# Performance work log

Hardware: AMD Instinct MI355X
Metric: run time of the kernel (lower is better)

## Reference

```python
import jax, jax.numpy as jnp
import numpy as np

N, E = 50000, 800000
D, H, C, ED = 128, 8, 16, 32  # in_channels, heads, head_dim, edge_dim
EPS = 1e-5

def _ln(x, g, b):
    mu = jnp.mean(x, axis=-1, keepdims=True)
    var = jnp.mean((x - mu) ** 2, axis=-1, keepdims=True)
    return (x - mu) * jax.lax.rsqrt(var + EPS) * g + b

def setup_inputs() -> dict:
    key = jax.random.key(0)
    ks = jax.random.split(key, 20)
    s = 0.05
    inp = {
        'x': jax.random.normal(ks[0], (N, D), jnp.float32),
        'edge_index': jax.random.randint(ks[1], (2, E), 0, N, jnp.int64),
        'edge_attr': jax.random.normal(ks[2], (E, ED), jnp.float32),
        'Wq': jax.random.normal(ks[3], (D, H * C)) * s,
        'bq': jnp.zeros((H * C,)),
        'Wk': jax.random.normal(ks[4], (D, H * C)) * s,
        'bk': jnp.zeros((H * C,)),
        'Wv': jax.random.normal(ks[5], (D, H * C)) * s,
        'bv': jnp.zeros((H * C,)),
        'We': jax.random.normal(ks[6], (ED, H * C)) * s,
        'Wskip': jax.random.normal(ks[7], (D, H * C)) * s,
        'bskip': jnp.zeros((H * C,)),
        'ln1_g': jnp.ones((D,)), 'ln1_b': jnp.zeros((D,)),
        'W1': jax.random.normal(ks[8], (D, 4 * D)) * s,
        'b1': jnp.zeros((4 * D,)),
        'W2': jax.random.normal(ks[9], (4 * D, D)) * s,
        'b2': jnp.zeros((D,)),
        'ln2_g': jnp.ones((D,)), 'ln2_b': jnp.zeros((D,)),
    }
    return inp

def reference(x, edge_index, edge_attr, Wq, bq, Wk, bk, Wv, bv, We, Wskip, bskip,
              ln1_g, ln1_b, W1, b1, W2, b2, ln2_g, ln2_b):
    src, dst = edge_index[0], edge_index[1]
    # node-level projections, then gather per-edge  [N,H,C] -> [E,H,C]
    q = (x @ Wq + bq).reshape(N, H, C)
    k = (x @ Wk + bk).reshape(N, H, C)
    v = (x @ Wv + bv).reshape(N, H, C)
    e = (edge_attr @ We).reshape(E, H, C)
    k_e = k[src] + e
    alpha = jnp.sum(q[dst] * k_e, axis=-1) / jnp.sqrt(jnp.float32(C))  # [E,H]
    # segment softmax over destination nodes
    m = jax.ops.segment_max(alpha, dst, num_segments=N)               # [N,H]
    p = jnp.exp(alpha - m[dst])
    denom = jax.ops.segment_sum(p, dst, num_segments=N)
    a = p / (denom[dst] + 1e-16)
    out_e = (v[src] + e) * a[..., None]                               # [E,H,C]
    attn = jax.ops.segment_sum(out_e, dst, num_segments=N).reshape(N, H * C)
    attn = attn + x @ Wskip + bskip  # root/skip connection
    # transformer block: residual + LN + FFN + LN (dropout = identity, eval)
    h = _ln(x + attn, ln1_g, ln1_b)
    ffn = jax.nn.relu(h @ W1 + b1) @ W2 + b2
    return _ln(h + ffn, ln2_g, ln2_b)
```

## Files before the change

kernel.cpp:

```cpp
#include <hip/hip_runtime.h>
#include <hip/hip_bf16.h>

using bf16 = __hip_bfloat16;
typedef __attribute__((ext_vector_type(8))) short short8;
typedef __attribute__((ext_vector_type(4))) float floatx4;

#define NN 50000
#define EE 800000
#define DD 128
#define HH 8
#define CC 16
#define EDD 32
#define DF 512
#define NQC 64
#define PART 782

__device__ __forceinline__ float b2f(bf16 v) { return __bfloat162float(v); }
__device__ __forceinline__ float bs2f(short s) {
    bf16 h = *reinterpret_cast<bf16*>(&s);
    return __bfloat162float(h);
}
__device__ __forceinline__ float bu2f(unsigned short s) {
    unsigned int u = ((unsigned int)s) << 16;
    return *reinterpret_cast<float*>(&u);
}
__device__ __forceinline__ short f2bs(float v) {
    bf16 h = __float2bfloat16(v);
    return *reinterpret_cast<short*>(&h);
}

__device__ __forceinline__ int clampn(int v)
{
    return (v < 0) ? 0 : (v >= NN ? NN - 1 : v);
}

__global__ void k_packall(const float* __restrict__ Wq, const float* __restrict__ Wk,
                          const float* __restrict__ Wv, const float* __restrict__ Wsk,
                          const float* __restrict__ W1, const float* __restrict__ W2,
                          const float* __restrict__ We,
                          bf16* __restrict__ wqp, bf16* __restrict__ wkp,
                          bf16* __restrict__ wvp, bf16* __restrict__ wskp,
                          bf16* __restrict__ w1p, bf16* __restrict__ w2p,
                          bf16* __restrict__ wep,
                          const int* __restrict__ ei, int* __restrict__ flag)
{
    int idx = blockIdx.x * 256 + threadIdx.x;
    const float* W; bf16* out; int ksteps, N, local;
    if (idx < 65536) {
        int wsel = idx >> 14; local = idx & 16383;
        W   = (wsel == 0) ? Wq  : (wsel == 1) ? Wk  : (wsel == 2) ? Wv  : Wsk;
        out = (wsel == 0) ? wqp : (wsel == 1) ? wkp : (wsel == 2) ? wvp : wskp;
        ksteps = 4; N = 128;
    } else if (idx < 131072) { local = idx - 65536;  W = W1; out = w1p; ksteps = 4;  N = 512; }
    else if (idx < 196608)   { local = idx - 131072; W = W2; out = w2p; ksteps = 16; N = 128; }
    else if (idx < 200704)   { local = idx - 196608; W = We; out = wep; ksteps = 1;  N = 128; }
    else {
        if (idx == 200704) {
            int all0 = 1;
            for (int i = 0; i < 16; ++i) all0 &= (ei[2 * i + 1] == 0);
            flag[0] = all0;
        }
        return;
    }
    int j = local & 7, lane = (local >> 3) & 63, rest = local >> 9;
    int kstep = rest % ksteps, ntile = rest / ksteps;
    int quad = lane >> 4, m = lane & 15;
    int k = kstep * 32 + quad * 8 + j;
    int n = ntile * 16 + m;
    out[local] = __float2bfloat16(W[(size_t)k * N + n]);
}

__global__ __launch_bounds__(256) void k_proj(
    const float* __restrict__ x,
    const bf16* __restrict__ wqp, const bf16* __restrict__ wkp,
    const bf16* __restrict__ wvp, const bf16* __restrict__ wskp,
    const float* __restrict__ bq, const float* __restrict__ bk,
    const float* __restrict__ bv, const float* __restrict__ bsk,
    bf16* __restrict__ qb, unsigned int* __restrict__ kvb,
    bf16* __restrict__ skipb)
{
    __shared__ __align__(16) short xs[32][136];
    __shared__ __align__(16) short os[32][520];
    const int t = threadIdx.x;
    const int wave = t >> 6, lane = t & 63;
    const int quad = lane >> 4, m = lane & 15;
    const int n0 = blockIdx.x * 32;

    for (int idx = t; idx < 32 * 32; idx += 256) {
        int row = idx >> 5, g = idx & 31;
        int node = n0 + row;
        float4 xv = {0.f, 0.f, 0.f, 0.f};
        if (node < NN) xv = *reinterpret_cast<const float4*>(&x[(size_t)node * 128 + g * 4]);
        short4 s4;
        s4.x = f2bs(xv.x); s4.y = f2bs(xv.y); s4.z = f2bs(xv.z); s4.w = f2bs(xv.w);
        *reinterpret_cast<short4*>(&xs[row][g * 4]) = s4;
    }
    __syncthreads();

    const bf16* Wp = (wave == 0) ? wqp : (wave == 1) ? wkp : (wave == 2) ? wvp : wskp;
    const float* bias = (wave == 0) ? bq : (wave == 1) ? bk : (wave == 2) ? bv : bsk;

    floatx4 acc[2][8];
#pragma unroll
    for (int mt = 0; mt < 2; ++mt)
#pragma unroll
        for (int nt = 0; nt < 8; ++nt) acc[mt][nt] = (floatx4){0.f, 0.f, 0.f, 0.f};

#pragma unroll
    for (int kstep = 0; kstep < 4; ++kstep) {
        short8 af0 = *reinterpret_cast<const short8*>(&xs[m][kstep * 32 + quad * 8]);
        short8 af1 = *reinterpret_cast<const short8*>(&xs[16 + m][kstep * 32 + quad * 8]);
#pragma unroll
        for (int nt = 0; nt < 8; ++nt) {
            short8 bf = *reinterpret_cast<const short8*>(
                reinterpret_cast<const short*>(Wp) + ((nt * 4 + kstep) * 64 + lane) * 8);
            acc[0][nt] = __builtin_amdgcn_mfma_f32_16x16x32_bf16(af0, bf, acc[0][nt], 0, 0, 0);
            acc[1][nt] = __builtin_amdgcn_mfma_f32_16x16x32_bf16(af1, bf, acc[1][nt], 0, 0, 0);
        }
    }
#pragma unroll
    for (int nt = 0; nt < 8; ++nt) {
        float bs = bias[nt * 16 + m];
#pragma unroll
        for (int mt = 0; mt < 2; ++mt)
#pragma unroll
            for (int r = 0; r < 4; ++r)
                os[mt * 16 + quad * 4 + r][wave * 128 + nt * 16 + m] = f2bs(acc[mt][nt][r] + bs);
    }
    __syncthreads();
    for (int idx = t; idx < 32 * 64; idx += 256) {
        int row = idx >> 6, c = idx & 63;
        int node = n0 + row;
        if (node >= NN) continue;
        unsigned int qu  = *reinterpret_cast<const unsigned int*>(&os[row][2 * c]);
        unsigned int ku  = *reinterpret_cast<const unsigned int*>(&os[row][128 + 2 * c]);
        unsigned int vu  = *reinterpret_cast<const unsigned int*>(&os[row][256 + 2 * c]);
        unsigned int sku = *reinterpret_cast<const unsigned int*>(&os[row][384 + 2 * c]);
        reinterpret_cast<unsigned int*>(qb)[(size_t)node * 64 + c] = qu;
        reinterpret_cast<unsigned int*>(skipb)[(size_t)node * 64 + c] = sku;
        uint2 kv;
        kv.x = (ku & 0xffffu) | (vu << 16);
        kv.y = (ku >> 16) | (vu & 0xffff0000u);
        reinterpret_cast<uint2*>(kvb)[(size_t)node * 64 + c] = kv;
    }
}

__global__ void k_hist(const int* __restrict__ ei, const int* __restrict__ flag,
                       int* __restrict__ deg)
{
    int tt = blockIdx.x * 256 + threadIdx.x;
    int i0 = tt * 2;
    if (i0 >= EE) return;
    int d0, d1;
    if (flag[0]) {
        int4 v = *reinterpret_cast<const int4*>(&ei[2 * EE + 2 * i0]);
        d0 = v.x; d1 = v.z;
    } else {
        int2 v = *reinterpret_cast<const int2*>(&ei[EE + i0]);
        d0 = v.x; d1 = v.y;
    }
    atomicAdd(&deg[clampn(d0)], 1);
    atomicAdd(&deg[clampn(d1)], 1);
}

__global__ __launch_bounds__(1024) void k_scan(const int* __restrict__ deg,
                                               int* __restrict__ rowstart)
{
    __shared__ int s[1024];
    const int t = threadIdx.x;
    const int CH = 49;
    int base = t * CH;
    int sum = 0;
    for (int i = 0; i < CH; i++) {
        int idx = base + i;
        if (idx < NN) sum += deg[idx];
    }
    s[t] = sum;
    __syncthreads();
    int own = sum;
    for (int off = 1; off < 1024; off <<= 1) {
        int v = (t >= off) ? s[t - off] : 0;
        __syncthreads();
        s[t] += v;
        __syncthreads();
    }
    int run = s[t] - own;
    for (int i = 0; i < CH; i++) {
        int idx = base + i;
        if (idx < NN) {
            rowstart[idx] = run;
            run += deg[idx];
        }
    }
    if (t == 0) rowstart[NN] = EE;
}

__global__ void k_scatter(const int* __restrict__ ei, const int* __restrict__ flag,
                          const int* __restrict__ rowstart,
                          int* __restrict__ cursor, int* __restrict__ srcs,
                          const float* __restrict__ ea,
                          short* __restrict__ eacsr)
{
    int i = blockIdx.x * 256 + threadIdx.x;
    if (i >= EE) return;
    int is64 = flag[0];
    int d = clampn(is64 ? ei[2 * EE + 2 * i] : ei[EE + i]);
    int s = clampn(is64 ? ei[2 * i] : ei[i]);
    int pos = rowstart[d] + atomicAdd(&cursor[d], 1);
    __builtin_nontemporal_store(s, &srcs[pos]);
    const float4* er = reinterpret_cast<const float4*>(ea + (size_t)i * 32);
    short8* dst = reinterpret_cast<short8*>(eacsr + (size_t)pos * 32);
#pragma unroll
    for (int g = 0; g < 4; ++g) {
        float4 a = er[2 * g], b = er[2 * g + 1];
        short8 o;
        o[0] = f2bs(a.x); o[1] = f2bs(a.y); o[2] = f2bs(a.z); o[3] = f2bs(a.w);
        o[4] = f2bs(b.x); o[5] = f2bs(b.y); o[6] = f2bs(b.z); o[7] = f2bs(b.w);
        __builtin_nontemporal_store(o, &dst[g]);
    }
}

__global__ __launch_bounds__(256) void k_attn(
    const float* __restrict__ x,
    const short* __restrict__ eacsr, const bf16* __restrict__ wep,
    const bf16* __restrict__ qb, const unsigned int* __restrict__ kvb,
    const bf16* __restrict__ skipb,
    const int* __restrict__ rowstart, const int* __restrict__ srcs,
    const float* __restrict__ ln1g, const float* __restrict__ ln1b,
    int* __restrict__ qcounter, bf16* __restrict__ hb)
{
    __shared__ __align__(16) short es[4][128][18];
    __shared__ __align__(16) short wes[4096];
    const int t = threadIdx.x;
    const int wave = t >> 6, lane = t & 63;
    const int quad = lane >> 4, m = lane & 15;

    for (int idx = t; idx < 512; idx += 256)
        *reinterpret_cast<short8*>(&wes[idx * 8]) =
            *reinterpret_cast<const short8*>(reinterpret_cast<const short*>(wep) + idx * 8);
    __syncthreads();

    short (*esw)[18] = es[wave];
    const float QS = 0.3606737602f;

    const int gw = blockIdx.x * 4 + wave;
    const int c  = gw & (NQC - 1);
    const int base = c * PART;
    const int cnt_c = (NN - base < PART) ? (NN - base) : PART;
    int* qc = qcounter + c * 16;

    for (;;) {
        int nl;
        if (lane == 0) nl = atomicAdd(qc, 4);
        nl = __builtin_amdgcn_readfirstlane(nl);
        if (nl >= cnt_c) break;
        const int nhi = (nl + 4 < cnt_c) ? nl + 4 : cnt_c;

        for (int ni = nl; ni < nhi; ++ni) {
            const int n = base + ni;

            unsigned int qp = reinterpret_cast<const unsigned int*>(qb)[(size_t)n * 64 + lane];
            float q0 = bu2f((unsigned short)(qp & 0xffffu)) * QS;
            float q1 = bu2f((unsigned short)(qp >> 16)) * QS;

            const int eoff = rowstart[n], eend = rowstart[n + 1];
            float lsum = 0.f, acc0 = 0.f, acc1 = 0.f;

            for (int p0 = eoff; p0 < eend; p0 += 16) {
                int pos = p0 + m;
                int pc = (pos < eend) ? pos : eoff;
                int sj_all = srcs[pc];

                short8 Af = *reinterpret_cast<const short8*>(eacsr + (size_t)pc * 32 + quad * 8);

                uint2 kvr[16];
#pragma unroll
                for (int j = 0; j < 16; ++j) {
                    int sj = __builtin_amdgcn_readlane(sj_all, j);
                    kvr[j] = reinterpret_cast<const uint2*>(kvb + (size_t)(unsigned)sj * 128)[lane];
                }

#pragma unroll
                for (int nt = 0; nt < 8; ++nt) {
                    short8 Bf = *reinterpret_cast<const short8*>(&wes[(nt * 64 + lane) * 8]);
                    floatx4 C = {0.f, 0.f, 0.f, 0.f};
                    C = __builtin_amdgcn_mfma_f32_16x16x32_bf16(Af, Bf, C, 0, 0, 0);
                    int col = nt * 16 + m;
                    unsigned int d0 = (unsigned int)(unsigned short)f2bs(C[0]) |
                                      ((unsigned int)(unsigned short)f2bs(C[1]) << 16);
                    unsigned int d1 = (unsigned int)(unsigned short)f2bs(C[2]) |
                                      ((unsigned int)(unsigned short)f2bs(C[3]) << 16);
                    unsigned int* p = reinterpret_cast<unsigned int*>(&esw[col][quad * 4]);
                    p[0] = d0; p[1] = d1;
                }
                __builtin_amdgcn_wave_barrier();

                unsigned int ear[8], ebr[8];
                {
                    const unsigned int* ra = reinterpret_cast<const unsigned int*>(&esw[2 * lane][0]);
                    const unsigned int* rb = reinterpret_cast<const unsigned int*>(&esw[2 * lane + 1][0]);
#pragma unroll
                    for (int jj = 0; jj < 8; ++jj) { ear[jj] = ra[jj]; ebr[jj] = rb[jj]; }
                }

                int cnt = eend - p0; if (cnt > 16) cnt = 16;
#pragma unroll
                for (int j = 0; j < 16; ++j) {
                    unsigned int eva = ear[j >> 1], evb = ebr[j >> 1];
                    float e0 = (j & 1) ? bu2f((unsigned short)(eva >> 16))
                                       : bu2f((unsigned short)(eva & 0xffffu));
                    float e1 = (j & 1) ? bu2f((unsigned short)(evb >> 16))
                                       : bu2f((unsigned short)(evb & 0xffffu));
                    float k0 = bu2f((unsigned short)(kvr[j].x & 0xffffu));
                    float v0 = bu2f((unsigned short)(kvr[j].x >> 16));
                    float k1 = bu2f((unsigned short)(kvr[j].y & 0xffffu));
                    float v1 = bu2f((unsigned short)(kvr[j].y >> 16));
                    float pr = fmaf(k1 + e1, q1, (k0 + e0) * q0);
                    pr += __int_as_float(__builtin_amdgcn_ds_swizzle(__float_as_int(pr), 0x041F));
                    pr += __int_as_float(__builtin_amdgcn_ds_swizzle(__float_as_int(pr), 0x081F));
                    pr += __int_as_float(__builtin_amdgcn_ds_swizzle(__float_as_int(pr), 0x101F));
                    float w = (j < cnt) ? __builtin_amdgcn_exp2f(pr) : 0.f;
                    lsum += w;
                    acc0 = fmaf(v0 + e0, w, acc0);
                    acc1 = fmaf(v1 + e1, w, acc1);
                }
                __builtin_amdgcn_wave_barrier();
            }

            float rden = 1.f / (lsum + 1e-16f);
            float attn0 = acc0 * rden, attn1 = acc1 * rden;
            float2 xv = *reinterpret_cast<const float2*>(x + (size_t)n * 128 + 2 * lane);
            unsigned int skp = reinterpret_cast<const unsigned int*>(skipb)[(size_t)n * 64 + lane];
            float pre0 = xv.x + attn0 + bu2f((unsigned short)(skp & 0xffffu));
            float pre1 = xv.y + attn1 + bu2f((unsigned short)(skp >> 16));
            float s1 = pre0 + pre1, s2 = pre0 * pre0 + pre1 * pre1;
#pragma unroll
            for (int off = 1; off < 64; off <<= 1) {
                s1 += __shfl_xor(s1, off);
                s2 += __shfl_xor(s2, off);
            }
            float mu = s1 * (1.f / 128.f);
            float var = s2 * (1.f / 128.f) - mu * mu;
            float inv = rsqrtf(var + 1e-5f);
            float2 g  = *reinterpret_cast<const float2*>(ln1g + 2 * lane);
            float2 bb = *reinterpret_cast<const float2*>(ln1b + 2 * lane);
            float h0 = (pre0 - mu) * inv * g.x + bb.x;
            float h1 = (pre1 - mu) * inv * g.y + bb.y;
            unsigned int hu = (unsigned int)(unsigned short)f2bs(h0) |
                              ((unsigned int)(unsigned short)f2bs(h1) << 16);
            reinterpret_cast<unsigned int*>(hb)[(size_t)n * 64 + lane] = hu;
        }
    }
}

__global__ __launch_bounds__(256) void k_ffn(
    const bf16* __restrict__ hb,
    const bf16* __restrict__ w1p, const float* __restrict__ b1,
    const bf16* __restrict__ w2p, const float* __restrict__ b2,
    const float* __restrict__ ln2g, const float* __restrict__ ln2b,
    float* __restrict__ out)
{
    __shared__ __align__(16) short hs[32][136];
    __shared__ __align__(16) short t1s[32][520];
    float* fs = reinterpret_cast<float*>(&t1s[0][0]);
    const int t = threadIdx.x;
    const int wave = t >> 6, lane = t & 63;
    const int quad = lane >> 4, m = lane & 15;
    const int n0 = blockIdx.x * 32;

    for (int idx = t; idx < 32 * 16; idx += 256) {
        int row = idx >> 4, g = idx & 15;
        int node = n0 + row;
        if (node < NN) {
            *reinterpret_cast<float4*>(&hs[row][g * 8]) =
                *reinterpret_cast<const float4*>(&hb[(size_t)node * 128 + g * 8]);
        } else {
            float4 z = {0.f, 0.f, 0.f, 0.f};
            *reinterpret_cast<float4*>(&hs[row][g * 8]) = z;
        }
    }
    __syncthreads();

    floatx4 acc1[2][8];
#pragma unroll
    for (int mt = 0; mt < 2; ++mt)
#pragma unroll
        for (int nt = 0; nt < 8; ++nt) acc1[mt][nt] = (floatx4){0.f, 0.f, 0.f, 0.f};
#pragma unroll
    for (int kstep = 0; kstep < 4; ++kstep) {
        short8 af0 = *reinterpret_cast<const short8*>(&hs[m][kstep * 32 + quad * 8]);
        short8 af1 = *reinterpret_cast<const short8*>(&hs[16 + m][kstep * 32 + quad * 8]);
#pragma unroll
        for (int nt = 0; nt < 8; ++nt) {
            short8 bf = *reinterpret_cast<const short8*>(
                reinterpret_cast<const short*>(w1p) + (((wave * 8 + nt) * 4 + kstep) * 64 + lane) * 8);
            acc1[0][nt] = __builtin_amdgcn_mfma_f32_16x16x32_bf16(af0, bf, acc1[0][nt], 0, 0, 0);
            acc1[1][nt] = __builtin_amdgcn_mfma_f32_16x16x32_bf16(af1, bf, acc1[1][nt], 0, 0, 0);
        }
    }
#pragma unroll
    for (int nt = 0; nt < 8; ++nt) {
        float bs = b1[wave * 128 + nt * 16 + m];
#pragma unroll
        for (int mt = 0; mt < 2; ++mt)
#pragma unroll
            for (int r = 0; r < 4; ++r)
                t1s[mt * 16 + quad * 4 + r][wave * 128 + nt * 16 + m] =
                    f2bs(fmaxf(acc1[mt][nt][r] + bs, 0.f));
    }
    __syncthreads();

    floatx4 acc2[2][2];
#pragma unroll
    for (int mt = 0; mt < 2; ++mt)
#pragma unroll
        for (int nt = 0; nt < 2; ++nt) acc2[mt][nt] = (floatx4){0.f, 0.f, 0.f, 0.f};
#pragma unroll
    for (int kstep = 0; kstep < 16; ++kstep) {
        short8 af0 = *reinterpret_cast<const short8*>(&t1s[m][kstep * 32 + quad * 8]);
        short8 af1 = *reinterpret_cast<const short8*>(&t1s[16 + m][kstep * 32 + quad * 8]);
#pragma unroll
        for (int nt = 0; nt < 2; ++nt) {
            short8 bf = *reinterpret_cast<const short8*>(
                reinterpret_cast<const short*>(w2p) + (((wave * 2 + nt) * 16 + kstep) * 64 + lane) * 8);
            acc2[0][nt] = __builtin_amdgcn_mfma_f32_16x16x32_bf16(af0, bf, acc2[0][nt], 0, 0, 0);
            acc2[1][nt] = __builtin_amdgcn_mfma_f32_16x16x32_bf16(af1, bf, acc2[1][nt], 0, 0, 0);
        }
    }
    __syncthreads();
#pragma unroll
    for (int nt = 0; nt < 2; ++nt) {
        int col = (wave * 2 + nt) * 16 + m;
        float bs = b2[col];
#pragma unroll
        for (int mt = 0; mt < 2; ++mt)
#pragma unroll
            for (int r = 0; r < 4; ++r)
                fs[(mt * 16 + quad * 4 + r) * 132 + col] = acc2[mt][nt][r] + bs;
    }
    __syncthreads();

    for (int rr = 0; rr < 8; ++rr) {
        int row = wave * 8 + rr;
        int node = n0 + row;
        float p0 = bs2f(hs[row][lane]) + fs[row * 132 + lane];
        float p1 = bs2f(hs[row][lane + 64]) + fs[row * 132 + lane + 64];
        float s1 = p0 + p1, s2 = p0 * p0 + p1 * p1;
#pragma unroll
        for (int off = 1; off < 64; off <<= 1) {
            s1 += __shfl_xor(s1, off);
            s2 += __shfl_xor(s2, off);
        }
        float mu = s1 * (1.f / 128.f);
        float var = s2 * (1.f / 128.f) - mu * mu;
        float inv = rsqrtf(var + 1e-5f);
        if (node < NN) {
            float o0 = (p0 - mu) * inv * ln2g[lane] + ln2b[lane];
            float o1 = (p1 - mu) * inv * ln2g[lane + 64] + ln2b[lane + 64];
            __builtin_nontemporal_store(o0, &out[(size_t)node * 128 + lane]);
            __builtin_nontemporal_store(o1, &out[(size_t)node * 128 + lane + 64]);
        }
    }
}

extern "C" void kernel_launch(void* const* d_in, const int* in_sizes, int n_in,
                              void* d_out, int out_size, void* d_ws, size_t ws_size,
                              hipStream_t stream)
{
    const float* x    = (const float*)d_in[0];
    const int*   ei   = (const int*)d_in[1];
    const float* ea   = (const float*)d_in[2];
    const float* Wq   = (const float*)d_in[3];
    const float* bq   = (const float*)d_in[4];
    const float* Wk   = (const float*)d_in[5];
    const float* bk   = (const float*)d_in[6];
    const float* Wv   = (const float*)d_in[7];
    const float* bv   = (const float*)d_in[8];
    const float* We   = (const float*)d_in[9];
    const float* Wsk  = (const float*)d_in[10];
    const float* bsk  = (const float*)d_in[11];
    const float* ln1g = (const float*)d_in[12];
    const float* ln1b = (const float*)d_in[13];
    const float* W1   = (const float*)d_in[14];
    const float* b1   = (const float*)d_in[15];
    const float* W2   = (const float*)d_in[16];
    const float* b2   = (const float*)d_in[17];
    const float* ln2g = (const float*)d_in[18];
    const float* ln2b = (const float*)d_in[19];

    char* ws = (char*)d_ws;
    size_t off = 0;
    auto alloc = [&](size_t bytes) -> void* {
        void* p = ws + off;
        off += (bytes + 255) & ~(size_t)255;
        return p;
    };
    int*   flag     = (int*)alloc(256);
    int*   qcounter = (int*)alloc((size_t)NQC * 16 * 4);
    int*   deg      = (int*)alloc((size_t)NN * 4);
    int*   cursor   = (int*)alloc((size_t)NN * 4);
    int*   rowstart = (int*)alloc((size_t)(NN + 1) * 4);
    int*   srcs     = (int*)alloc((size_t)EE * 4);
    short* eacsr    = (short*)alloc((size_t)EE * 32 * 2);
    bf16*  qb       = (bf16*)alloc((size_t)NN * 128 * 2);
    unsigned int* kvb = (unsigned int*)alloc((size_t)NN * 128 * 4);
    bf16*  skipb    = (bf16*)alloc((size_t)NN * 128 * 2);
    bf16*  hb       = (bf16*)alloc((size_t)NN * 128 * 2);
    bf16*  wqp      = (bf16*)alloc((size_t)16384 * 2);
    bf16*  wkp      = (bf16*)alloc((size_t)16384 * 2);
    bf16*  wvp      = (bf16*)alloc((size_t)16384 * 2);
    bf16*  wskp     = (bf16*)alloc((size_t)16384 * 2);
    bf16*  w1p      = (bf16*)alloc((size_t)65536 * 2);
    bf16*  w2p      = (bf16*)alloc((size_t)65536 * 2);
    bf16*  wep      = (bf16*)alloc((size_t)4096 * 2);

    hipMemsetAsync(deg, 0, (size_t)NN * 4, stream);
    hipMemsetAsync(cursor, 0, (size_t)NN * 4, stream);
    hipMemsetAsync(qcounter, 0, (size_t)NQC * 16 * 4, stream);

    k_packall<<<785, 256, 0, stream>>>(
        Wq, Wk, Wv, Wsk, W1, W2, We, wqp, wkp, wvp, wskp, w1p, w2p, wep, ei, flag);
    k_hist<<<(EE / 2 + 255) / 256, 256, 0, stream>>>(ei, flag, deg);
    k_proj<<<(NN + 31) / 32, 256, 0, stream>>>(x, wqp, wkp, wvp, wskp,
                                               bq, bk, bv, bsk, qb, kvb, skipb);
    k_scan<<<1, 1024, 0, stream>>>(deg, rowstart);
    k_scatter<<<(EE + 255) / 256, 256, 0, stream>>>(ei, flag, rowstart, cursor,
                                                    srcs, ea, eacsr);
    k_attn<<<1536, 256, 0, stream>>>(x, eacsr, wep, qb, kvb, skipb,
                                     rowstart, srcs, ln1g, ln1b, qcounter, hb);
    k_ffn<<<(NN + 31) / 32, 256, 0, stream>>>(hb, w1p, b1, w2p, b2, ln2g, ln2b, (float*)d_out);
}
```

Measured before the change: 634.4 us.

## Drop CSR edge_attr copy, gather fp32 edge features by edge id in attention

The scatter kernel no longer converts and permutes edge_attr into a bf16 CSR buffer. It now stores a (src, edge id) pair per CSR slot, and the attention kernel reads fp32 edge_attr rows indirectly and converts them to bf16 in registers. This removes a full write and read of a 51 MB intermediate, but attention now makes scattered 128-byte fp32 reads instead of contiguous 64-byte bf16 reads. The x residual is also folded into the skip buffer inside k_proj, the three memsets move into k_packall, and the non-temporal output stores become plain stores.

After: 547.7 us. 1.16x faster.

```diff
diff --git a/kernel.cpp b/kernel.cpp
--- a/kernel.cpp
+++ b/kernel.cpp
@@ -42,9 +42,15 @@
                           bf16* __restrict__ wvp, bf16* __restrict__ wskp,
                           bf16* __restrict__ w1p, bf16* __restrict__ w2p,
                           bf16* __restrict__ wep,
-                          const int* __restrict__ ei, int* __restrict__ flag)
+                          const int* __restrict__ ei, int* __restrict__ flag,
+                          int* __restrict__ deg, int* __restrict__ cursor,
+                          int* __restrict__ qcounter)
 {
     int idx = blockIdx.x * 256 + threadIdx.x;
+    if (idx < NN) deg[idx] = 0;
+    else if (idx < 2 * NN) cursor[idx - NN] = 0;
+    else if (idx < 2 * NN + NQC * 16) qcounter[idx - 2 * NN] = 0;
+
     const float* W; bf16* out; int ksteps, N, local;
     if (idx < 65536) {
         int wsel = idx >> 14; local = idx & 16383;
@@ -135,7 +141,10 @@
         unsigned int qu  = *reinterpret_cast<const unsigned int*>(&os[row][2 * c]);
         unsigned int ku  = *reinterpret_cast<const unsigned int*>(&os[row][128 + 2 * c]);
         unsigned int vu  = *reinterpret_cast<const unsigned int*>(&os[row][256 + 2 * c]);
-        unsigned int sku = *reinterpret_cast<const unsigned int*>(&os[row][384 + 2 * c]);
+        float sk0 = bs2f(os[row][384 + 2 * c])     + bs2f(xs[row][2 * c]);
+        float sk1 = bs2f(os[row][384 + 2 * c + 1]) + bs2f(xs[row][2 * c + 1]);
+        unsigned int sku = (unsigned int)(unsigned short)f2bs(sk0) |
+                           ((unsigned int)(unsigned short)f2bs(sk1) << 16);
         reinterpret_cast<unsigned int*>(qb)[(size_t)node * 64 + c] = qu;
         reinterpret_cast<unsigned int*>(skipb)[(size_t)node * 64 + c] = sku;
         uint2 kv;
@@ -197,9 +206,7 @@
 
 __global__ void k_scatter(const int* __restrict__ ei, const int* __restrict__ flag,
                           const int* __restrict__ rowstart,
-                          int* __restrict__ cursor, int* __restrict__ srcs,
-                          const float* __restrict__ ea,
-                          short* __restrict__ eacsr)
+                          int* __restrict__ cursor, int2* __restrict__ srcid)
 {
     int i = blockIdx.x * 256 + threadIdx.x;
     if (i >= EE) return;
@@ -207,25 +214,14 @@
     int d = clampn(is64 ? ei[2 * EE + 2 * i] : ei[EE + i]);
     int s = clampn(is64 ? ei[2 * i] : ei[i]);
     int pos = rowstart[d] + atomicAdd(&cursor[d], 1);
-    __builtin_nontemporal_store(s, &srcs[pos]);
-    const float4* er = reinterpret_cast<const float4*>(ea + (size_t)i * 32);
-    short8* dst = reinterpret_cast<short8*>(eacsr + (size_t)pos * 32);
-#pragma unroll
-    for (int g = 0; g < 4; ++g) {
-        float4 a = er[2 * g], b = er[2 * g + 1];
-        short8 o;
-        o[0] = f2bs(a.x); o[1] = f2bs(a.y); o[2] = f2bs(a.z); o[3] = f2bs(a.w);
-        o[4] = f2bs(b.x); o[5] = f2bs(b.y); o[6] = f2bs(b.z); o[7] = f2bs(b.w);
-        __builtin_nontemporal_store(o, &dst[g]);
-    }
+    srcid[pos] = make_int2(s, i);
 }
 
 __global__ __launch_bounds__(256) void k_attn(
-    const float* __restrict__ x,
-    const short* __restrict__ eacsr, const bf16* __restrict__ wep,
+    const float* __restrict__ edge_attr, const bf16* __restrict__ wep,
     const bf16* __restrict__ qb, const unsigned int* __restrict__ kvb,
     const bf16* __restrict__ skipb,
-    const int* __restrict__ rowstart, const int* __restrict__ srcs,
+    const int* __restrict__ rowstart, const int2* __restrict__ srcid,
     const float* __restrict__ ln1g, const float* __restrict__ ln1b,
     int* __restrict__ qcounter, bf16* __restrict__ hb)
 {
@@ -269,17 +265,22 @@
             for (int p0 = eoff; p0 < eend; p0 += 16) {
                 int pos = p0 + m;
                 int pc = (pos < eend) ? pos : eoff;
-                int sj_all = srcs[pc];
-
-                short8 Af = *reinterpret_cast<const short8*>(eacsr + (size_t)pc * 32 + quad * 8);
+                int2 se = srcid[pc];
+
+                const float* arow = edge_attr + (size_t)se.y * 32 + quad * 8;
+                float4 a0 = *reinterpret_cast<const float4*>(arow);
+                float4 a1 = *reinterpret_cast<const float4*>(arow + 4);
 
                 uint2 kvr[16];
 #pragma unroll
                 for (int j = 0; j < 16; ++j) {
-                    int sj = __builtin_amdgcn_readlane(sj_all, j);
+                    int sj = __builtin_amdgcn_readlane(se.x, j);
                     kvr[j] = reinterpret_cast<const uint2*>(kvb + (size_t)(unsigned)sj * 128)[lane];
                 }
 
+                short8 Af;
+                Af[0] = f2bs(a0.x); Af[1] = f2bs(a0.y); Af[2] = f2bs(a0.z); Af[3] = f2bs(a0.w);
+                Af[4] = f2bs(a1.x); Af[5] = f2bs(a1.y); Af[6] = f2bs(a1.z); Af[7] = f2bs(a1.w);
 #pragma unroll
                 for (int nt = 0; nt < 8; ++nt) {
                     short8 Bf = *reinterpret_cast<const short8*>(&wes[(nt * 64 + lane) * 8]);
@@ -329,10 +330,9 @@
 
             float rden = 1.f / (lsum + 1e-16f);
             float attn0 = acc0 * rden, attn1 = acc1 * rden;
-            float2 xv = *reinterpret_cast<const float2*>(x + (size_t)n * 128 + 2 * lane);
             unsigned int skp = reinterpret_cast<const unsigned int*>(skipb)[(size_t)n * 64 + lane];
-            float pre0 = xv.x + attn0 + bu2f((unsigned short)(skp & 0xffffu));
-            float pre1 = xv.y + attn1 + bu2f((unsigned short)(skp >> 16));
+            float pre0 = attn0 + bu2f((unsigned short)(skp & 0xffffu));
+            float pre1 = attn1 + bu2f((unsigned short)(skp >> 16));
             float s1 = pre0 + pre1, s2 = pre0 * pre0 + pre1 * pre1;
 #pragma unroll
             for (int off = 1; off < 64; off <<= 1) {
@@ -455,10 +455,8 @@
         float var = s2 * (1.f / 128.f) - mu * mu;
         float inv = rsqrtf(var + 1e-5f);
         if (node < NN) {
-            float o0 = (p0 - mu) * inv * ln2g[lane] + ln2b[lane];
-            float o1 = (p1 - mu) * inv * ln2g[lane + 64] + ln2b[lane + 64];
-            __builtin_nontemporal_store(o0, &out[(size_t)node * 128 + lane]);
-            __builtin_nontemporal_store(o1, &out[(size_t)node * 128 + lane + 64]);
+            out[(size_t)node * 128 + lane] = (p0 - mu) * inv * ln2g[lane] + ln2b[lane];
+            out[(size_t)node * 128 + lane + 64] = (p1 - mu) * inv * ln2g[lane + 64] + ln2b[lane + 64];
         }
     }
 }
@@ -500,8 +498,7 @@
     int*   deg      = (int*)alloc((size_t)NN * 4);
     int*   cursor   = (int*)alloc((size_t)NN * 4);
     int*   rowstart = (int*)alloc((size_t)(NN + 1) * 4);
-    int*   srcs     = (int*)alloc((size_t)EE * 4);
-    short* eacsr    = (short*)alloc((size_t)EE * 32 * 2);
+    int2*  srcid    = (int2*)alloc((size_t)EE * 8);
     bf16*  qb       = (bf16*)alloc((size_t)NN * 128 * 2);
     unsigned int* kvb = (unsigned int*)alloc((size_t)NN * 128 * 4);
     bf16*  skipb    = (bf16*)alloc((size_t)NN * 128 * 2);
@@ -514,19 +511,15 @@
     bf16*  w2p      = (bf16*)alloc((size_t)65536 * 2);
     bf16*  wep      = (bf16*)alloc((size_t)4096 * 2);
 
-    hipMemsetAsync(deg, 0, (size_t)NN * 4, stream);
-    hipMemsetAsync(cursor, 0, (size_t)NN * 4, stream);
-    hipMemsetAsync(qcounter, 0, (size_t)NQC * 16 * 4, stream);
-
     k_packall<<<785, 256, 0, stream>>>(
-        Wq, Wk, Wv, Wsk, W1, W2, We, wqp, wkp, wvp, wskp, w1p, w2p, wep, ei, flag);
+        Wq, Wk, Wv, Wsk, W1, W2, We, wqp, wkp, wvp, wskp, w1p, w2p, wep,
+        ei, flag, deg, cursor, qcounter);
     k_hist<<<(EE / 2 + 255) / 256, 256, 0, stream>>>(ei, flag, deg);
     k_proj<<<(NN + 31) / 32, 256, 0, stream>>>(x, wqp, wkp, wvp, wskp,
                                                bq, bk, bv, bsk, qb, kvb, skipb);
     k_scan<<<1, 1024, 0, stream>>>(deg, rowstart);
-    k_scatter<<<(EE + 255) / 256, 256, 0, stream>>>(ei, flag, rowstart, cursor,
-                                                    srcs, ea, eacsr);
-    k_attn<<<1536, 256, 0, stream>>>(x, eacsr, wep, qb, kvb, skipb,
-                                     rowstart, srcs, ln1g, ln1b, qcounter, hb);
+    k_scatter<<<(EE + 255) / 256, 256, 0, stream>>>(ei, flag, rowstart, cursor, srcid);
+    k_attn<<<1536, 256, 0, stream>>>(ea, wep, qb, kvb, skipb,
+                                     rowstart, srcid, ln1g, ln1b, qcounter, hb);
     k_ffn<<<(NN + 31) / 32, 256, 0, stream>>>(hb, w1p, b1, w2p, b2, ln2g, ln2b, (float*)d_out);
 }
```
